# Kernel tuning notes

Measured on AMD Instinct MI355X. Metric: run time of the kernel, lower is better.

Reference implementation:

```python
import jax, jax.numpy as jnp
import numpy as np

N = 100000
E = 1600000
NEG_SLOPE = 0.2
DEPTH = 5


def setup_inputs() -> dict:
    key = jax.random.key(0)
    ks = jax.random.split(key, 8)
    x = jax.random.normal(ks[0], (N, 100), dtype=jnp.float32)
    edge_index = jax.random.randint(ks[1], (2, E), 0, N, dtype=jnp.int64)
    # layer 0: 100 -> 48; layers 1..4: 48 -> 48
    W0 = jax.random.normal(ks[2], (100, 48), dtype=jnp.float32) * 0.1
    Wrest = jax.random.normal(ks[3], (DEPTH - 1, 48, 48), dtype=jnp.float32) * 0.1
    a_src = jax.random.normal(ks[4], (DEPTH, 48), dtype=jnp.float32) * 0.1
    a_dst = jax.random.normal(ks[5], (DEPTH, 48), dtype=jnp.float32) * 0.1
    bias = jax.random.normal(ks[6], (DEPTH, 48), dtype=jnp.float32) * 0.1
    return {"x": x, "edge_index": edge_index, "W0": W0, "Wrest": Wrest,
            "a_src": a_src, "a_dst": a_dst, "bias": bias}


def _gat_layer(x, src, dst, W, a_s, a_d, b):
    h = x @ W                                   # [N, F]
    alpha_s = h @ a_s                           # [N]
    alpha_d = h @ a_d                           # [N]
    e = alpha_s[src] + alpha_d[dst]             # [E']
    e = jax.nn.leaky_relu(e, NEG_SLOPE)
    # segment softmax over edges grouped by destination node
    m = jax.ops.segment_max(e, dst, num_segments=N)
    m = jnp.where(jnp.isfinite(m), m, 0.0)      # empty segments -> 0
    p = jnp.exp(e - m[dst])
    s = jax.ops.segment_sum(p, dst, num_segments=N)
    alpha = p / jnp.maximum(s[dst], 1e-16)      # [E']
    out = jax.ops.segment_sum(alpha[:, None] * h[src], dst, num_segments=N)
    return out + b


def reference(x, edge_index, W0, Wrest, a_src, a_dst, bias):
    # PyG GATConv default add_self_loops=True
    loops = jnp.arange(N, dtype=edge_index.dtype)
    src = jnp.concatenate([edge_index[0], loops])
    dst = jnp.concatenate([edge_index[1], loops])
    Ws = [W0] + [Wrest[i] for i in range(DEPTH - 1)]
    h = x
    for l in range(DEPTH):
        h = _gat_layer(h, src, dst, Ws[l], a_src[l], a_dst[l], bias[l])
        h = jax.nn.elu(h)
    return h
```

## Files before the change

### kernel.cpp

```cpp
#include <hip/hip_runtime.h>

#define NN 100000
#define EE 1600000
#define ETOT (EE + NN)
#define FF 48
#define NEG 0.2f
#define BSH 9
#define BNODES 512
#define NBUK ((NN + BNODES - 1) / BNODES)
#define TILE 2048


__global__ __launch_bounds__(256) void k_bhist(const int* __restrict__ ei,
                                               int* __restrict__ bcnt) {
    __shared__ int h[256];
    int t = threadIdx.x;
    h[t] = 0;
    __syncthreads();
    for (int i = blockIdx.x * 256 + t; i < ETOT; i += gridDim.x * 256) {
        int dd = (i < EE) ? ei[EE + i] : (i - EE);
        atomicAdd(&h[dd >> BSH], 1);
    }
    __syncthreads();
    if (h[t] > 0) atomicAdd(&bcnt[t], h[t]);
}

__global__ void k_bscan(const int* __restrict__ bcnt, int* __restrict__ boff,
                        int* __restrict__ bcur) {
    __shared__ int sb[256];
    int t = threadIdx.x;
    int v = (t < NBUK) ? bcnt[t] : 0;
    sb[t] = v;
    __syncthreads();
    for (int o = 1; o < 256; o <<= 1) {
        int x = (t >= o) ? sb[t - o] : 0;
        __syncthreads();
        sb[t] += x;
        __syncthreads();
    }
    int excl = sb[t] - v;
    boff[t] = excl;
    bcur[t] = excl;
}

__global__ __launch_bounds__(256) void k_bscatter(const int* __restrict__ ei,
                                                  int* __restrict__ bcur,
                                                  int2* __restrict__ pairs) {
    __shared__ int hist[256], incl[256], exc[256], curv[256], gb[256];
    __shared__ int2 stage[TILE];
    __shared__ int staddr[TILE];
    int t = threadIdx.x;
    hist[t] = 0;
    __syncthreads();
    int base = blockIdx.x * TILE;
    int s[8], d[8], b[8];
#pragma unroll
    for (int j = 0; j < 8; j++) {
        int i = base + t + j * 256;
        if (i < ETOT) {
            int ss, dd;
            if (i < EE) { ss = ei[i]; dd = ei[EE + i]; }
            else { ss = i - EE; dd = ss; }
            s[j] = ss; d[j] = dd; b[j] = dd >> BSH;
            atomicAdd(&hist[b[j]], 1);
        } else {
            b[j] = -1;
        }
    }
    __syncthreads();
    int hv = hist[t];
    incl[t] = hv;
    __syncthreads();
    for (int o = 1; o < 256; o <<= 1) {
        int x = (t >= o) ? incl[t - o] : 0;
        __syncthreads();
        incl[t] += x;
        __syncthreads();
    }
    int excl = incl[t] - hv;
    exc[t] = excl;
    curv[t] = excl;
    if (hv > 0) gb[t] = atomicAdd(&bcur[t], hv);
    __syncthreads();
    int total = incl[255];
#pragma unroll
    for (int j = 0; j < 8; j++) {
        if (b[j] >= 0) {
            int pos = atomicAdd(&curv[b[j]], 1);
            stage[pos] = make_int2(s[j], d[j]);
            staddr[pos] = gb[b[j]] + (pos - exc[b[j]]);
        }
    }
    __syncthreads();
    for (int i = t; i < total; i += 256) pairs[staddr[i]] = stage[i];
}

__global__ __launch_bounds__(256) void k_bfill(const int2* __restrict__ pairs,
                                               const int* __restrict__ boff,
                                               int* __restrict__ off,
                                               int* __restrict__ ssrc) {
    __shared__ int cnt[BNODES], cu[BNODES], sb[256];
    int blk = blockIdx.x;
    int t = threadIdx.x;
    int n0 = blk << BSH;
    int beg = boff[blk], end = boff[blk + 1];
    cnt[t] = 0;
    cnt[t + 256] = 0;
    __syncthreads();
    for (int i = beg + t; i < end; i += 256) {
        atomicAdd(&cnt[pairs[i].y - n0], 1);
    }
    __syncthreads();
    int c0 = cnt[2 * t], c1 = cnt[2 * t + 1];
    sb[t] = c0 + c1;
    __syncthreads();
    for (int o = 1; o < 256; o <<= 1) {
        int x = (t >= o) ? sb[t - o] : 0;
        __syncthreads();
        sb[t] += x;
        __syncthreads();
    }
    int e2 = sb[t] - (c0 + c1);
    cu[2 * t] = e2;
    cu[2 * t + 1] = e2 + c0;
    int n1 = min(n0 + BNODES, NN);
    if (n0 + 2 * t < n1) off[n0 + 2 * t] = beg + e2;
    if (n0 + 2 * t + 1 < n1) off[n0 + 2 * t + 1] = beg + e2 + c0;
    if (blk == 0 && t == 0) off[NN] = ETOT;
    __syncthreads();
    for (int i = beg + t; i < end; i += 256) {
        int2 pr = pairs[i];
        int pos = atomicAdd(&cu[pr.y - n0], 1);
        ssrc[beg + pos] = pr.x;
    }
}


template <int K, int KC, int R>
__global__ __launch_bounds__(256) void k_gemm(const float* __restrict__ in,
                                              const float* __restrict__ W,
                                              const float* __restrict__ a_s,
                                              const float* __restrict__ a_d,
                                              float* __restrict__ h,
                                              float* __restrict__ as_,
                                              float* __restrict__ ad_) {
    __shared__ float Wl[K * FF];
    __shared__ float asl[FF], adl[FF];
    int t = threadIdx.x;
    for (int i = t; i < K * FF / 4; i += 256)
        ((float4*)Wl)[i] = ((const float4*)W)[i];
    if (t < FF) { asl[t] = a_s[t]; adl[t] = a_d[t]; }
    __syncthreads();

    int fg = t & 3;
    int pr = t >> 2;
    int r0 = blockIdx.x * (64 * R) + pr * R;
    if (r0 >= NN) return;

    constexpr int NC = K / KC;
    constexpr int QC = KC / 4;
    const float4* x4 = (const float4*)in;
    const float4* wl4 = (const float4*)Wl;

    float acc[R][12];
#pragma unroll
    for (int r = 0; r < R; r++)
#pragma unroll
        for (int j = 0; j < 12; j++) acc[r][j] = 0.f;

    for (int c = 0; c < NC; c++) {
        float xs[R][KC];
#pragma unroll
        for (int r = 0; r < R; r++) {
#pragma unroll
            for (int q = 0; q < QC; q++) {
                float4 v = x4[(size_t)(r0 + r) * (K / 4) + c * QC + q];
                xs[r][4 * q + 0] = v.x; xs[r][4 * q + 1] = v.y;
                xs[r][4 * q + 2] = v.z; xs[r][4 * q + 3] = v.w;
            }
        }
#pragma unroll
        for (int kk = 0; kk < KC; kk++) {
            const int k = c * KC + kk;
            const float4 w0 = wl4[k * 12 + fg * 3 + 0];
            const float4 w1 = wl4[k * 12 + fg * 3 + 1];
            const float4 w2 = wl4[k * 12 + fg * 3 + 2];
#pragma unroll
            for (int r = 0; r < R; r++) {
                const float xv = xs[r][kk];
                acc[r][0] = fmaf(xv, w0.x, acc[r][0]);
                acc[r][1] = fmaf(xv, w0.y, acc[r][1]);
                acc[r][2] = fmaf(xv, w0.z, acc[r][2]);
                acc[r][3] = fmaf(xv, w0.w, acc[r][3]);
                acc[r][4] = fmaf(xv, w1.x, acc[r][4]);
                acc[r][5] = fmaf(xv, w1.y, acc[r][5]);
                acc[r][6] = fmaf(xv, w1.z, acc[r][6]);
                acc[r][7] = fmaf(xv, w1.w, acc[r][7]);
                acc[r][8] = fmaf(xv, w2.x, acc[r][8]);
                acc[r][9] = fmaf(xv, w2.y, acc[r][9]);
                acc[r][10] = fmaf(xv, w2.z, acc[r][10]);
                acc[r][11] = fmaf(xv, w2.w, acc[r][11]);
            }
        }
    }

#pragma unroll
    for (int r = 0; r < R; r++) {
        float4* hp = (float4*)(h + (size_t)(r0 + r) * FF + fg * 12);
        hp[0] = make_float4(acc[r][0], acc[r][1], acc[r][2], acc[r][3]);
        hp[1] = make_float4(acc[r][4], acc[r][5], acc[r][6], acc[r][7]);
        hp[2] = make_float4(acc[r][8], acc[r][9], acc[r][10], acc[r][11]);
    }

    float ps[R], pd[R];
#pragma unroll
    for (int r = 0; r < R; r++) { ps[r] = 0.f; pd[r] = 0.f; }
#pragma unroll
    for (int j = 0; j < 12; j++) {
        float av = asl[fg * 12 + j], dv = adl[fg * 12 + j];
#pragma unroll
        for (int r = 0; r < R; r++) {
            ps[r] = fmaf(acc[r][j], av, ps[r]);
            pd[r] = fmaf(acc[r][j], dv, pd[r]);
        }
    }
#pragma unroll
    for (int r = 0; r < R; r++) {
        ps[r] += __shfl_xor(ps[r], 1); ps[r] += __shfl_xor(ps[r], 2);
        pd[r] += __shfl_xor(pd[r], 1); pd[r] += __shfl_xor(pd[r], 2);
    }
    if (fg == 0) {
#pragma unroll
        for (int r = 0; r < R; r++) {
            as_[r0 + r] = ps[r];
            ad_[r0 + r] = pd[r];
        }
    }
}

template <bool LAST>
__global__ __launch_bounds__(256) void k_aggr_fused(
    const float* __restrict__ h, const float* __restrict__ as_,
    const float* __restrict__ ad_, const int* __restrict__ off,
    const int* __restrict__ ssrc, const float* __restrict__ bias_l,
    const float* __restrict__ Wn, const float* __restrict__ asn,
    const float* __restrict__ adn, float* __restrict__ hn,
    float* __restrict__ as_o, float* __restrict__ ad_o,
    float* __restrict__ out) {
    int wave = threadIdx.x >> 6;
    int lane = threadIdx.x & 63;
    int gid = blockIdx.x * 4 + wave;
    if (gid * 4 >= NN) return;
    int fW = (lane < FF) ? lane : lane - FF;
    unsigned foff = (unsigned)(fW * 4);
    const char* hb = (const char*)h;
    float bias_v = bias_l[fW];

    float w[48];
    float asn_v = 0.f, adn_v = 0.f;
    if (!LAST) {
        asn_v = asn[fW];
        adn_v = adn[fW];
#pragma unroll
        for (int k = 0; k < 48; k++) w[k] = Wn[k * FF + fW];
    }

    for (int n = 0; n < 4; n++) {
        int d = gid * 4 + n;
        int beg = __builtin_amdgcn_readfirstlane(off[d]);
        int end = __builtin_amdgcn_readfirstlane(off[d + 1]);
        int deg = end - beg;
        float add = ad_[d];

        float acc = 0.f, s = 0.f;

        if (deg <= 64) {
            int srcb = 0;
            float e = -1e30f;
            if (lane < deg) {
                int src = ssrc[beg + lane];
                srcb = src * (FF * 4);
                float t = as_[src] + add;
                e = (t > 0.f) ? t : NEG * t;
            }
            float m = e;
#pragma unroll
            for (int o = 32; o; o >>= 1) m = fmaxf(m, __shfl_xor(m, o));
            float p = (lane < deg) ? __expf(e - m) : 0.f;
            float sv = p;
#pragma unroll
            for (int o = 32; o; o >>= 1) sv += __shfl_xor(sv, o);
            s = sv;

            unsigned pbits = __float_as_uint(p);
            int degR = (deg + 7) & ~7;
            for (int i = 0; i < degR; i += 8) {
                float pj[8], hv[8];
#pragma unroll
                for (int j = 0; j < 8; j++) {
                    pj[j] = __uint_as_float(
                        (unsigned)__builtin_amdgcn_readlane((int)pbits, i + j));
                    int sbj = __builtin_amdgcn_readlane(srcb, i + j);
                    hv[j] = *(const float*)(hb + (unsigned)sbj + foff);
                }
#pragma unroll
                for (int j = 0; j < 8; j++) acc = fmaf(pj[j], hv[j], acc);
            }
        } else {
            float m = -1e30f;
            for (int i = beg + lane; i < end; i += 64) {
                float t = as_[ssrc[i]] + add;
                t = (t > 0.f) ? t : NEG * t;
                m = fmaxf(m, t);
            }
#pragma unroll
            for (int o = 32; o; o >>= 1) m = fmaxf(m, __shfl_xor(m, o));
            for (int i = beg; i < end; i++) {
                int src = ssrc[i];
                float e = as_[src] + add;
                e = (e > 0.f) ? e : NEG * e;
                float pp = __expf(e - m);
                s += pp;
                if (lane < FF) acc = fmaf(pp, h[(size_t)src * FF + lane], acc);
            }
        }

        float v = acc / fmaxf(s, 1e-16f) + bias_v;
        float act = (v > 0.f) ? v : (__expf(v) - 1.0f);

        if (LAST) {
            if (lane < FF) out[(size_t)d * FF + lane] = act;
            continue;
        }

        float c0 = 0.f, c1 = 0.f, c2 = 0.f, c3 = 0.f;
        int ab = __float_as_int(act);
#pragma unroll
        for (int k = 0; k < 12; k++) {
            float a0 = __uint_as_float((unsigned)__builtin_amdgcn_readlane(ab, k));
            float a1 = __uint_as_float((unsigned)__builtin_amdgcn_readlane(ab, 12 + k));
            float a2 = __uint_as_float((unsigned)__builtin_amdgcn_readlane(ab, 24 + k));
            float a3 = __uint_as_float((unsigned)__builtin_amdgcn_readlane(ab, 36 + k));
            c0 = fmaf(a0, w[k], c0);
            c1 = fmaf(a1, w[12 + k], c1);
            c2 = fmaf(a2, w[24 + k], c2);
            c3 = fmaf(a3, w[36 + k], c3);
        }
        float hn_acc = (c0 + c1) + (c2 + c3);

        float hz = (lane < FF) ? hn_acc : 0.f;
        float ps = hz * asn_v;
        float pd = hz * adn_v;
#pragma unroll
        for (int o = 32; o; o >>= 1) {
            ps += __shfl_xor(ps, o);
            pd += __shfl_xor(pd, o);
        }

        if (lane < FF) hn[(size_t)d * FF + lane] = hn_acc;
        if (lane == 0) { as_o[d] = ps; ad_o[d] = pd; }
    }
}


static inline size_t alup(size_t x) { return (x + 255) & ~(size_t)255; }

extern "C" void kernel_launch(void* const* d_in, const int* in_sizes, int n_in,
                              void* d_out, int out_size, void* d_ws, size_t ws_size,
                              hipStream_t stream) {
    const float* x = (const float*)d_in[0];
    const int* ei = (const int*)d_in[1];
    const float* W0 = (const float*)d_in[2];
    const float* Wr = (const float*)d_in[3];
    const float* As = (const float*)d_in[4];
    const float* Ad = (const float*)d_in[5];
    const float* B = (const float*)d_in[6];
    float* out = (float*)d_out;

    char* p = (char*)d_ws;
    int* off = (int*)p;      p += alup((NN + 1) * sizeof(int));
    int* bcnt = (int*)p;     p += alup(256 * sizeof(int));
    int* boff = (int*)p;     p += alup(257 * sizeof(int));
    int* bcur = (int*)p;     p += alup(256 * sizeof(int));
    int2* pairs = (int2*)p;  p += alup((size_t)ETOT * sizeof(int2));
    int* ssrc = (int*)p;     p += alup((size_t)ETOT * sizeof(int) + 256);
    float* hA = (float*)p;   p += alup((size_t)NN * FF * sizeof(float) + 256);
    float* hB = (float*)p;   p += alup((size_t)NN * FF * sizeof(float) + 256);
    float* asA = (float*)p;  p += alup(NN * sizeof(float));
    float* adA = (float*)p;  p += alup(NN * sizeof(float));
    float* asB = (float*)p;  p += alup(NN * sizeof(float));
    float* adB = (float*)p;  p += alup(NN * sizeof(float));

    hipMemsetAsync(bcnt, 0, 256 * sizeof(int), stream);
    k_bhist<<<512, 256, 0, stream>>>(ei, bcnt);
    k_bscan<<<1, 256, 0, stream>>>(bcnt, boff, bcur);
    k_bscatter<<<(ETOT + TILE - 1) / TILE, 256, 0, stream>>>(ei, bcur, pairs);
    k_bfill<<<NBUK, 256, 0, stream>>>(pairs, boff, off, ssrc);

    int g0 = (NN + 127) / 128;
    k_gemm<100, 20, 2><<<g0, 256, 0, stream>>>(x, W0, As, Ad, hA, asA, adA);

    int gA = (NN + 15) / 16;
    k_aggr_fused<false><<<gA, 256, 0, stream>>>(hA, asA, adA, off, ssrc, B + 0,
                                                Wr + 0 * 2304, As + 48, Ad + 48,
                                                hB, asB, adB, nullptr);
    k_aggr_fused<false><<<gA, 256, 0, stream>>>(hB, asB, adB, off, ssrc, B + 48,
                                                Wr + 1 * 2304, As + 96, Ad + 96,
                                                hA, asA, adA, nullptr);
    k_aggr_fused<false><<<gA, 256, 0, stream>>>(hA, asA, adA, off, ssrc, B + 96,
                                                Wr + 2 * 2304, As + 144, Ad + 144,
                                                hB, asB, adB, nullptr);
    k_aggr_fused<false><<<gA, 256, 0, stream>>>(hB, asB, adB, off, ssrc, B + 144,
                                                Wr + 3 * 2304, As + 192, Ad + 192,
                                                hA, asA, adA, nullptr);
    k_aggr_fused<true><<<gA, 256, 0, stream>>>(hA, asA, adA, off, ssrc, B + 192,
                                               nullptr, nullptr, nullptr,
                                               nullptr, nullptr, nullptr, out);
}
```

Before: 487.2 us.

## Process one destination node per wave and broadcast activations via LDS

```diff
diff --git a/kernel.cpp b/kernel.cpp
--- a/kernel.cpp
+++ b/kernel.cpp
@@ -247,10 +247,11 @@
     const float* __restrict__ adn, float* __restrict__ hn,
     float* __restrict__ as_o, float* __restrict__ ad_o,
     float* __restrict__ out) {
+    __shared__ float actl[4][64];
     int wave = threadIdx.x >> 6;
     int lane = threadIdx.x & 63;
-    int gid = blockIdx.x * 4 + wave;
-    if (gid * 4 >= NN) return;
+    int d = blockIdx.x * 4 + wave;
+    if (d >= NN) return;
     int fW = (lane < FF) ? lane : lane - FF;
     unsigned foff = (unsigned)(fW * 4);
     const char* hb = (const char*)h;
@@ -265,101 +266,111 @@
         for (int k = 0; k < 48; k++) w[k] = Wn[k * FF + fW];
     }
 
-    for (int n = 0; n < 4; n++) {
-        int d = gid * 4 + n;
-        int beg = __builtin_amdgcn_readfirstlane(off[d]);
-        int end = __builtin_amdgcn_readfirstlane(off[d + 1]);
-        int deg = end - beg;
-        float add = ad_[d];
-
-        float acc = 0.f, s = 0.f;
-
-        if (deg <= 64) {
-            int srcb = 0;
-            float e = -1e30f;
-            if (lane < deg) {
-                int src = ssrc[beg + lane];
-                srcb = src * (FF * 4);
-                float t = as_[src] + add;
-                e = (t > 0.f) ? t : NEG * t;
+    int beg = __builtin_amdgcn_readfirstlane(off[d]);
+    int end = __builtin_amdgcn_readfirstlane(off[d + 1]);
+    int deg = end - beg;
+    float add = ad_[d];
+
+    float acc = 0.f, s = 0.f;
+
+    if (deg <= 64) {
+        int srcb = 0;
+        float e = -1e30f;
+        if (lane < deg) {
+            int src = ssrc[beg + lane];
+            srcb = src * (FF * 4);
+            float t = as_[src] + add;
+            e = (t > 0.f) ? t : NEG * t;
+        }
+        float m = e;
+#pragma unroll
+        for (int o = 32; o; o >>= 1) m = fmaxf(m, __shfl_xor(m, o));
+        float p = (lane < deg) ? __expf(e - m) : 0.f;
+        float sv = p;
+#pragma unroll
+        for (int o = 32; o; o >>= 1) sv += __shfl_xor(sv, o);
+        s = sv;
+
+        unsigned pbits = __float_as_uint(p);
+        int degR = (deg + 7) & ~7;
+        for (int i = 0; i < degR; i += 8) {
+            float pj[8], hv[8];
+#pragma unroll
+            for (int j = 0; j < 8; j++) {
+                pj[j] = __uint_as_float(
+                    (unsigned)__builtin_amdgcn_readlane((int)pbits, i + j));
+                int sbj = __builtin_amdgcn_readlane(srcb, i + j);
+                hv[j] = *(const float*)(hb + (unsigned)sbj + foff);
             }
-            float m = e;
-#pragma unroll
-            for (int o = 32; o; o >>= 1) m = fmaxf(m, __shfl_xor(m, o));
-            float p = (lane < deg) ? __expf(e - m) : 0.f;
-            float sv = p;
-#pragma unroll
-            for (int o = 32; o; o >>= 1) sv += __shfl_xor(sv, o);
-            s = sv;
-
-            unsigned pbits = __float_as_uint(p);
-            int degR = (deg + 7) & ~7;
-            for (int i = 0; i < degR; i += 8) {
-                float pj[8], hv[8];
-#pragma unroll
-                for (int j = 0; j < 8; j++) {
-                    pj[j] = __uint_as_float(
-                        (unsigned)__builtin_amdgcn_readlane((int)pbits, i + j));
-                    int sbj = __builtin_amdgcn_readlane(srcb, i + j);
-                    hv[j] = *(const float*)(hb + (unsigned)sbj + foff);
-                }
-#pragma unroll
-                for (int j = 0; j < 8; j++) acc = fmaf(pj[j], hv[j], acc);
-            }
-        } else {
-            float m = -1e30f;
-            for (int i = beg + lane; i < end; i += 64) {
-                float t = as_[ssrc[i]] + add;
-                t = (t > 0.f) ? t : NEG * t;
-                m = fmaxf(m, t);
-            }
-#pragma unroll
-            for (int o = 32; o; o >>= 1) m = fmaxf(m, __shfl_xor(m, o));
-            for (int i = beg; i < end; i++) {
-                int src = ssrc[i];
-                float e = as_[src] + add;
-                e = (e > 0.f) ? e : NEG * e;
-                float pp = __expf(e - m);
-                s += pp;
-                if (lane < FF) acc = fmaf(pp, h[(size_t)src * FF + lane], acc);
-            }
-        }
-
-        float v = acc / fmaxf(s, 1e-16f) + bias_v;
-        float act = (v > 0.f) ? v : (__expf(v) - 1.0f);
-
-        if (LAST) {
-            if (lane < FF) out[(size_t)d * FF + lane] = act;
-            continue;
-        }
-
-        float c0 = 0.f, c1 = 0.f, c2 = 0.f, c3 = 0.f;
-        int ab = __float_as_int(act);
-#pragma unroll
-        for (int k = 0; k < 12; k++) {
-            float a0 = __uint_as_float((unsigned)__builtin_amdgcn_readlane(ab, k));
-            float a1 = __uint_as_float((unsigned)__builtin_amdgcn_readlane(ab, 12 + k));
-            float a2 = __uint_as_float((unsigned)__builtin_amdgcn_readlane(ab, 24 + k));
-            float a3 = __uint_as_float((unsigned)__builtin_amdgcn_readlane(ab, 36 + k));
-            c0 = fmaf(a0, w[k], c0);
-            c1 = fmaf(a1, w[12 + k], c1);
-            c2 = fmaf(a2, w[24 + k], c2);
-            c3 = fmaf(a3, w[36 + k], c3);
-        }
-        float hn_acc = (c0 + c1) + (c2 + c3);
-
-        float hz = (lane < FF) ? hn_acc : 0.f;
-        float ps = hz * asn_v;
-        float pd = hz * adn_v;
-#pragma unroll
-        for (int o = 32; o; o >>= 1) {
-            ps += __shfl_xor(ps, o);
-            pd += __shfl_xor(pd, o);
-        }
-
-        if (lane < FF) hn[(size_t)d * FF + lane] = hn_acc;
-        if (lane == 0) { as_o[d] = ps; ad_o[d] = pd; }
-    }
+#pragma unroll
+            for (int j = 0; j < 8; j++) acc = fmaf(pj[j], hv[j], acc);
+        }
+    } else {
+        float m = -1e30f;
+        for (int i = beg + lane; i < end; i += 64) {
+            float t = as_[ssrc[i]] + add;
+            t = (t > 0.f) ? t : NEG * t;
+            m = fmaxf(m, t);
+        }
+#pragma unroll
+        for (int o = 32; o; o >>= 1) m = fmaxf(m, __shfl_xor(m, o));
+        for (int i = beg; i < end; i++) {
+            int src = ssrc[i];
+            float e = as_[src] + add;
+            e = (e > 0.f) ? e : NEG * e;
+            float pp = __expf(e - m);
+            s += pp;
+            if (lane < FF) acc = fmaf(pp, h[(size_t)src * FF + lane], acc);
+        }
+    }
+
+    float v = acc / fmaxf(s, 1e-16f) + bias_v;
+    float act = (v > 0.f) ? v : (__expf(v) - 1.0f);
+
+    if (LAST) {
+        if (lane < FF) out[(size_t)d * FF + lane] = act;
+        return;
+    }
+
+    actl[wave][lane] = act;
+    const float4* a4 = (const float4*)&actl[wave][0];
+    float c0 = 0.f, c1 = 0.f, c2 = 0.f, c3 = 0.f;
+#pragma unroll
+    for (int q = 0; q < 3; q++) {
+        float4 v0 = a4[q];
+        float4 v1 = a4[3 + q];
+        float4 v2 = a4[6 + q];
+        float4 v3 = a4[9 + q];
+        c0 = fmaf(v0.x, w[4 * q + 0], c0);
+        c0 = fmaf(v0.y, w[4 * q + 1], c0);
+        c0 = fmaf(v0.z, w[4 * q + 2], c0);
+        c0 = fmaf(v0.w, w[4 * q + 3], c0);
+        c1 = fmaf(v1.x, w[12 + 4 * q + 0], c1);
+        c1 = fmaf(v1.y, w[12 + 4 * q + 1], c1);
+        c1 = fmaf(v1.z, w[12 + 4 * q + 2], c1);
+        c1 = fmaf(v1.w, w[12 + 4 * q + 3], c1);
+        c2 = fmaf(v2.x, w[24 + 4 * q + 0], c2);
+        c2 = fmaf(v2.y, w[24 + 4 * q + 1], c2);
+        c2 = fmaf(v2.z, w[24 + 4 * q + 2], c2);
+        c2 = fmaf(v2.w, w[24 + 4 * q + 3], c2);
+        c3 = fmaf(v3.x, w[36 + 4 * q + 0], c3);
+        c3 = fmaf(v3.y, w[36 + 4 * q + 1], c3);
+        c3 = fmaf(v3.z, w[36 + 4 * q + 2], c3);
+        c3 = fmaf(v3.w, w[36 + 4 * q + 3], c3);
+    }
+    float hn_acc = (c0 + c1) + (c2 + c3);
+
+    float hz = (lane < FF) ? hn_acc : 0.f;
+    float ps = hz * asn_v;
+    float pd = hz * adn_v;
+#pragma unroll
+    for (int o = 32; o; o >>= 1) {
+        ps += __shfl_xor(ps, o);
+        pd += __shfl_xor(pd, o);
+    }
+
+    if (lane < FF) hn[(size_t)d * FF + lane] = hn_acc;
+    if (lane == 0) { as_o[d] = ps; ad_o[d] = pd; }
 }
 
 
@@ -400,7 +411,7 @@
     int g0 = (NN + 127) / 128;
     k_gemm<100, 20, 2><<<g0, 256, 0, stream>>>(x, W0, As, Ad, hA, asA, adA);
 
-    int gA = (NN + 15) / 16;
+    int gA = (NN + 3) / 4;
     k_aggr_fused<false><<<gA, 256, 0, stream>>>(hA, asA, adA, off, ssrc, B + 0,
                                                 Wr + 0 * 2304, As + 48, Ad + 48,
                                                 hB, asB, adB, nullptr);
```

Result: slower. 520.9 us (+6.9%).
